# Kernel tuning notes

Measured on AMD Instinct MI355X. Metric: run time of the kernel, lower is better.

## Reference

```python
import jax, jax.numpy as jnp
from jax import lax
import numpy as np

B, CIN, CP, H, W = 16, 64, 64, 64, 64
K1 = 3   # deformable kernel
K2 = 5   # parallel conv kernel
EPS = 1e-5


def conv2d(x, w, stride, pad):
    return lax.conv_general_dilated(
        x, w, (stride, stride), [(pad, pad), (pad, pad)],
        dimension_numbers=('NCHW', 'OIHW', 'NCHW'))


def batchnorm(x, g, b, m, v):
    scale = g / jnp.sqrt(v + EPS)
    return (x - m[None, :, None, None]) * scale[None, :, None, None] + b[None, :, None, None]


def deform_conv2d(x, offset, weight, stride, pad):
    # x: [B,Cin,H,W], offset: [B,2*K*K,Ho,Wo] (dy,dx interleaved per kernel tap, torchvision layout)
    Bn, Cin, Hn, Wn = x.shape
    Cout, _, K, _ = weight.shape
    KK = K * K
    Ho, Wo = offset.shape[2], offset.shape[3]
    off = offset.reshape(Bn, KK, 2, Ho, Wo)
    dy, dx = off[:, :, 0], off[:, :, 1]                      # [B,KK,Ho,Wo]
    ky, kx = jnp.meshgrid(jnp.arange(K), jnp.arange(K), indexing='ij')
    ky = ky.reshape(KK).astype(x.dtype)
    kx = kx.reshape(KK).astype(x.dtype)
    base_y = (jnp.arange(Ho) * stride - pad).astype(x.dtype)
    base_x = (jnp.arange(Wo) * stride - pad).astype(x.dtype)
    ys = base_y[None, None, :, None] + ky[None, :, None, None] + dy  # [B,KK,Ho,Wo]
    xs = base_x[None, None, None, :] + kx[None, :, None, None] + dx
    y0 = jnp.floor(ys); x0 = jnp.floor(xs)
    wy1 = ys - y0; wx1 = xs - x0
    wy0 = 1.0 - wy1; wx0 = 1.0 - wx1
    flat = x.reshape(Bn, Cin, Hn * Wn)

    def gather(yi, xi):
        valid = ((yi >= 0) & (yi <= Hn - 1) & (xi >= 0) & (xi <= Wn - 1))
        yc = jnp.clip(yi, 0, Hn - 1).astype(jnp.int32)
        xc = jnp.clip(xi, 0, Wn - 1).astype(jnp.int32)
        idx = (yc * Wn + xc).reshape(Bn, -1)                 # [B,KK*Ho*Wo]
        g = jax.vmap(lambda f, i: jnp.take(f, i, axis=1))(flat, idx)
        g = g.reshape(Bn, Cin, KK, Ho, Wo)
        return g * valid.astype(x.dtype)[:, None]

    val = (gather(y0, x0) * (wy0 * wx0)[:, None]
           + gather(y0, x0 + 1) * (wy0 * wx1)[:, None]
           + gather(y0 + 1, x0) * (wy1 * wx0)[:, None]
           + gather(y0 + 1, x0 + 1) * (wy1 * wx1)[:, None])   # [B,Cin,KK,Ho,Wo]
    w_r = weight.reshape(Cout, Cin, KK)
    return jnp.einsum('bcknm,ock->bonm', val, w_r)


def setup_inputs():
    key = jax.random.key(0)
    ks = jax.random.split(key, 18)
    f32 = jnp.float32
    x = jax.random.normal(ks[0], (B, CIN, H, W), f32)
    w_off = jax.random.normal(ks[1], (2 * K1 * K1, CIN, 3, 3), f32) * 0.01
    b_off = jnp.zeros((2 * K1 * K1,), f32)
    w1 = jax.random.normal(ks[2], (CP, CIN, K1, K1), f32) / np.sqrt(CIN * K1 * K1)
    w3 = jax.random.normal(ks[3], (CP, CIN, K2, K2), f32) / np.sqrt(CIN * K2 * K2)
    w2 = jax.random.normal(ks[4], (CP, CP, 3, 3), f32) / np.sqrt(CP * 9)
    def bn(i):
        g = jax.random.uniform(ks[5 + 4 * i], (CP,), f32, 0.5, 1.5)
        b = jax.random.normal(ks[6 + 4 * i], (CP,), f32) * 0.1
        m = jax.random.normal(ks[7 + 4 * i], (CP,), f32) * 0.1
        v = jax.random.uniform(ks[8 + 4 * i], (CP,), f32, 0.5, 1.5)
        return g, b, m, v
    g1, b1, m1, v1 = bn(0)
    g3, b3, m3, v3 = bn(1)
    g2, b2, m2, v2 = bn(2)
    return dict(x=x, w_off=w_off, b_off=b_off, w1=w1, g1=g1, b1=b1, m1=m1, v1=v1,
                w3=w3, g3=g3, b3=b3, m3=m3, v3=v3, w2=w2, g2=g2, b2=b2, m2=m2, v2=v2)


def reference(x, w_off, b_off, w1, g1, b1, m1, v1, w3, g3, b3, m3, v3, w2, g2, b2, m2, v2):
    offset1 = conv2d(x, w_off, 1, 1) + b_off[None, :, None, None]
    out = jax.nn.relu(batchnorm(deform_conv2d(x, offset1, w1, 1, 1), g1, b1, m1, v1))
    out_1 = jax.nn.relu(batchnorm(conv2d(x, w3, 1, 2), g3, b3, m3, v3))
    out = out + out_1
    out = batchnorm(conv2d(out, w2, 1, 1), g2, b2, m2, v2)
    out = out + x  # identity shortcut (stride=1, in_planes==planes)
    return jax.nn.relu(out)
```

## Files before the change

### kernel.cpp

```cpp
#include <hip/hip_runtime.h>
#include <hip/hip_bf16.h>


#define EPSv 1e-5f
#define XP 68

typedef _Float16 f16x2 __attribute__((ext_vector_type(2)));
typedef _Float16 f16x8 __attribute__((ext_vector_type(8)));
typedef __attribute__((ext_vector_type(16))) float f32x16;

__device__ inline ushort f2h(float f) {
  _Float16 h = (_Float16)f;
  return *(ushort*)&h;
}

__global__ __launch_bounds__(256) void prep_kernel(
    const float* __restrict__ x, const float* __restrict__ w3,
    const float* __restrict__ w2, const float* __restrict__ w1,
    const float* __restrict__ w_off,
    ushort* __restrict__ xTp, ushort* __restrict__ w3F,
    ushort* __restrict__ w2F, ushort* __restrict__ w1F,
    ushort* __restrict__ wofF) {
  __shared__ float tile[64][65];
  const int blk = blockIdx.x;
  if (blk < 1024) {
    const int y = blk & 63, b = blk >> 6;
    for (int i = threadIdx.x; i < 4096; i += 256) {
      int ci = i >> 6, xx = i & 63;
      tile[ci][xx] = x[(((size_t)b * 64 + ci) * 64 + y) * 64 + xx];
    }
    __syncthreads();
    for (int i = threadIdx.x; i < 2048; i += 256) {
      int xx = i >> 5, cip = (i & 31) * 2;
      ushort2 v;
      v.x = f2h(tile[cip][xx]);
      v.y = f2h(tile[cip + 1][xx]);
      *(ushort2*)&xTp[(((size_t)(b * 64 + y) * XP) + (xx + 2)) * 64 + cip] = v;
    }
    if (threadIdx.x < 128) {
      int colid = threadIdx.x >> 5;
      int col = (colid & 1) + (colid >> 1) * 66;
      int cip = (threadIdx.x & 31) * 2;
      ushort2 z; z.x = 0; z.y = 0;
      *(ushort2*)&xTp[(((size_t)(b * 64 + y) * XP) + col) * 64 + cip] = z;
    }
    return;
  }
  int idx = (blk - 1024) * 256 + threadIdx.x;
  if (idx < 102400) {
    int j = idx & 7, lane = (idx >> 3) & 63, ks = (idx >> 9) & 3;
    int half = (idx >> 11) & 1, kk = idx >> 12;
    int ln = lane & 31, kh = lane >> 5;
    int co = half * 32 + ln, ci = ks * 16 + kh * 8 + j;
    w3F[idx] = f2h(w3[(co * 64 + ci) * 25 + kk]);
    return;
  }
  idx -= 102400;
  if (idx < 36864) {
    int j = idx & 7, lane = (idx >> 3) & 63, ks = (idx >> 9) & 3;
    int half = (idx >> 11) & 1, kk = idx >> 12;
    int ln = lane & 31, kh = lane >> 5;
    int co = half * 32 + ln, ci = ks * 16 + kh * 8 + j;
    w2F[idx] = f2h(w2[(co * 64 + ci) * 9 + kk]);
    return;
  }
  idx -= 36864;
  if (idx < 36864) {
    int j = idx & 7, lane = (idx >> 3) & 63, ks = (idx >> 9) & 3;
    int half = (idx >> 11) & 1, kk = idx >> 12;
    int ln = lane & 31, kh = lane >> 5;
    int co = half * 32 + ln, ci = ks * 16 + kh * 8 + j;
    w1F[idx] = f2h(w1[(co * 64 + ci) * 9 + kk]);
    return;
  }
  idx -= 36864;
  if (idx < 18432) {
    int j = idx & 7, lane = (idx >> 3) & 63, ks = (idx >> 9) & 3;
    int kk = idx >> 11;
    int ln = lane & 31, kh = lane >> 5;
    int ci = ks * 16 + kh * 8 + j;
    wofF[idx] = f2h(ln < 18 ? w_off[(ln * 64 + ci) * 9 + kk] : 0.f);
  }
}

__device__ __forceinline__ f16x8 blend4(f16x8 va, f16x8 vb, f16x8 vc, f16x8 vd,
                                        f16x2 w00, f16x2 w01, f16x2 w10, f16x2 w11) {
  const f16x2* a = (const f16x2*)&va;
  const f16x2* b = (const f16x2*)&vb;
  const f16x2* c = (const f16x2*)&vc;
  const f16x2* d = (const f16x2*)&vd;
  f16x8 f;
  f16x2* fo = (f16x2*)&f;
#pragma unroll
  for (int i = 0; i < 4; ++i)
    fo[i] = a[i] * w00 + b[i] * w01 + c[i] * w10 + d[i] * w11;
  return f;
}

__global__ __launch_bounds__(256, 2) void fused_kernel(
    const ushort* __restrict__ xTp, const ushort* __restrict__ wofF,
    const float* __restrict__ b_off, const ushort* __restrict__ w1F,
    const ushort* __restrict__ w3F,
    const float* __restrict__ g1, const float* __restrict__ b1,
    const float* __restrict__ m1, const float* __restrict__ v1,
    const float* __restrict__ g3, const float* __restrict__ b3,
    const float* __restrict__ m3, const float* __restrict__ v3,
    ushort* __restrict__ s1T) {
  __shared__ __align__(16) uint4 ldsx[6 * 68 * 8];
  __shared__ float bn1s[64], bn1b[64], bn3s[64], bn3b[64];

  const int tid = threadIdx.x;
  const int wv = tid >> 6, lane = tid & 63;
  const int ln = lane & 31, kh = lane >> 5;
  const int r = wv >> 1, nt = wv & 1;
  const int y0 = blockIdx.x * 2, b = blockIdx.y;
  const int y = y0 + r, px = nt * 32 + ln;
  const uint4* xT4 = (const uint4*)xTp;
  const ushort* xb = xTp + (size_t)b * 64 * XP * 64;
  const bool interior = (y0 >= 2 && y0 <= 60);

  if (tid < 64) {
    float s = g1[tid] * rsqrtf(v1[tid] + EPSv);
    bn1s[tid] = s; bn1b[tid] = b1[tid] - m1[tid] * s;
    float s3 = g3[tid] * rsqrtf(v3[tid] + EPSv);
    bn3s[tid] = s3; bn3b[tid] = b3[tid] - m3[tid] * s3;
  }
  for (int i = tid; i < 6 * 68 * 8; i += 256) {
    int tr = i / (68 * 8), rem = i % (68 * 8);
    int col = rem >> 3, c = rem & 7;
    int ysrc = min(max(y0 - 2 + tr, 0), 63);
    uint4 v = xT4[((size_t)((b * 64 + ysrc) * XP + col)) * 8 + c];
    ldsx[(tr * 68 + col) * 8 + (c ^ (col & 7))] = v;
  }
  __syncthreads();

  f32x16 acco;
#pragma unroll
  for (int j = 0; j < 16; ++j) acco[j] = 0.f;
  if (interior) {
#pragma unroll
    for (int kk = 0; kk < 9; ++kk) {
      const int ky = kk / 3, kx = kk % 3;
      const int tr = r + ky + 1;
      const int col = px + kx + 1;
      f16x8 af[4], bf[4];
#pragma unroll
      for (int ks = 0; ks < 4; ++ks)
        af[ks] = *(const f16x8*)&wofF[(size_t)((kk * 4 + ks) * 64 + lane) * 8];
#pragma unroll
      for (int ks = 0; ks < 4; ++ks) {
        int c = ks * 2 + kh;
        bf[ks] = *(const f16x8*)&ldsx[(tr * 68 + col) * 8 + (c ^ (col & 7))];
      }
#pragma unroll
      for (int ks = 0; ks < 4; ++ks)
        acco = __builtin_amdgcn_mfma_f32_32x32x16_f16(af[ks], bf[ks], acco, 0, 0, 0);
    }
  } else {
#pragma unroll
    for (int kk = 0; kk < 9; ++kk) {
      const int ky = kk / 3, kx = kk % 3;
      const int yy = y - 1 + ky;
      if (yy >= 0 && yy <= 63) {
        const int tr = yy - (y0 - 2);
        const int col = px + kx + 1;
#pragma unroll
        for (int ks = 0; ks < 4; ++ks) {
          int c = ks * 2 + kh;
          f16x8 af = *(const f16x8*)&wofF[(size_t)((kk * 4 + ks) * 64 + lane) * 8];
          f16x8 bf = *(const f16x8*)&ldsx[(tr * 68 + col) * 8 + (c ^ (col & 7))];
          acco = __builtin_amdgcn_mfma_f32_32x32x16_f16(af, bf, acco, 0, 0, 0);
        }
      }
    }
  }
  float oth[10];
#pragma unroll
  for (int t = 0; t < 10; ++t) oth[t] = __shfl_xor(acco[t], 32);
  float dyv[9], dxv[9];
#pragma unroll
  for (int kk = 0; kk < 9; ++kk) {
    const int cY = 2 * kk, cX = 2 * kk + 1;
    const int rY = (cY & 3) + 4 * (cY >> 3);
    const int rX = (cX & 3) + 4 * (cX >> 3);
    const int sY = (cY >> 2) & 1, sX = (cX >> 2) & 1;
    float vy = (sY == kh) ? acco[rY] : oth[rY];
    float vx = (sX == kh) ? acco[rX] : oth[rX];
    dyv[kk] = vy + b_off[cY];
    dxv[kk] = vx + b_off[cX];
  }
  bool fast = true;
#pragma unroll
  for (int kk = 0; kk < 9; ++kk) {
    int iy0 = (int)floorf((float)(y - 1 + kk / 3) + dyv[kk]);
    int iy1 = iy0 + 1;
    bool ok0 = (iy0 < 0) || (iy0 > 63) || (iy0 >= y0 - 2 && iy0 <= y0 + 3);
    bool ok1 = (iy1 < 0) || (iy1 > 63) || (iy1 >= y0 - 2 && iy1 <= y0 + 3);
    fast = fast && ok0 && ok1;
  }
  const bool allfast = (__ballot(!fast) == 0ull);

  f32x16 accd0, accd1, acc50, acc51;
#pragma unroll
  for (int j = 0; j < 16; ++j) {
    accd0[j] = 0.f; accd1[j] = 0.f; acc50[j] = 0.f; acc51[j] = 0.f;
  }

  if (interior && allfast) {
#pragma unroll
    for (int dk = 0; dk < 9; ++dk) {
      {
        const int ky = dk / 3, kx = dk % 3;
        float ys = (float)(y - 1 + ky) + dyv[dk];
        float xs = (float)(px - 1 + kx) + dxv[dk];
        float y0f = floorf(ys), x0f = floorf(xs);
        float wy1 = ys - y0f, wx1 = xs - x0f;
        float wy0 = 1.f - wy1, wx0 = 1.f - wx1;
        int iy0 = (int)y0f, ix0 = (int)x0f;
        int iy1 = iy0 + 1, ix1 = ix0 + 1;
        float vy0 = (iy0 >= 0 && iy0 <= 63) ? 1.f : 0.f;
        float vy1 = (iy1 >= 0 && iy1 <= 63) ? 1.f : 0.f;
        float vx0 = (ix0 >= 0 && ix0 <= 63) ? 1.f : 0.f;
        float vx1 = (ix1 >= 0 && ix1 <= 63) ? 1.f : 0.f;
        int x0c = min(max(ix0, 0), 63), x1c = min(max(ix1, 0), 63);
        float w00 = wy0 * wx0 * vy0 * vx0;
        float w01 = wy0 * wx1 * vy0 * vx1;
        float w10 = wy1 * wx0 * vy1 * vx0;
        float w11 = wy1 * wx1 * vy1 * vx1;
        int tr0 = min(max(iy0 - (y0 - 2), 0), 5);
        int tr1 = min(max(iy1 - (y0 - 2), 0), 5);
        int c0 = x0c + 2, c1 = x1c + 2;
        f16x2 w00v = {(_Float16)w00, (_Float16)w00};
        f16x2 w01v = {(_Float16)w01, (_Float16)w01};
        f16x2 w10v = {(_Float16)w10, (_Float16)w10};
        f16x2 w11v = {(_Float16)w11, (_Float16)w11};

        f16x8 a0[4], a1[4], va[4], vb[4], vc[4], vd[4];
#pragma unroll
        for (int ks = 0; ks < 4; ++ks) {
          a0[ks] = *(const f16x8*)&w1F[(size_t)(((dk * 2 + 0) * 4 + ks) * 64 + lane) * 8];
          a1[ks] = *(const f16x8*)&w1F[(size_t)(((dk * 2 + 1) * 4 + ks) * 64 + lane) * 8];
        }
#pragma unroll
        for (int ks = 0; ks < 4; ++ks) {
          int c = ks * 2 + kh;
          va[ks] = *(const f16x8*)&ldsx[(tr0 * 68 + c0) * 8 + (c ^ (c0 & 7))];
          vb[ks] = *(const f16x8*)&ldsx[(tr0 * 68 + c1) * 8 + (c ^ (c1 & 7))];
          vc[ks] = *(const f16x8*)&ldsx[(tr1 * 68 + c0) * 8 + (c ^ (c0 & 7))];
          vd[ks] = *(const f16x8*)&ldsx[(tr1 * 68 + c1) * 8 + (c ^ (c1 & 7))];
        }
#pragma unroll
        for (int ks = 0; ks < 4; ++ks) {
          f16x8 f = blend4(va[ks], vb[ks], vc[ks], vd[ks], w00v, w01v, w10v, w11v);
          accd0 = __builtin_amdgcn_mfma_f32_32x32x16_f16(a0[ks], f, accd0, 0, 0, 0);
          accd1 = __builtin_amdgcn_mfma_f32_32x32x16_f16(a1[ks], f, accd1, 0, 0, 0);
        }
      }
      const int n5 = (dk < 7) ? 3 : 2;
      const int b5 = (dk < 7) ? dk * 3 : 21 + (dk - 7) * 2;
#pragma unroll
      for (int t = 0; t < 3; ++t) {
        if (t < n5) {
          const int kk = b5 + t;
          const int ky5 = kk / 5, kx5 = kk % 5;
          const int tr = r + ky5;
          const int col = px + kx5;
          f16x8 a0[4], a1[4], bfv[4];
#pragma unroll
          for (int ks = 0; ks < 4; ++ks) {
            a0[ks] = *(const f16x8*)&w3F[(size_t)(((kk * 2 + 0) * 4 + ks) * 64 + lane) * 8];
            a1[ks] = *(const f16x8*)&w3F[(size_t)(((kk * 2 + 1) * 4 + ks) * 64 + lane) * 8];
          }
#pragma unroll
          for (int ks = 0; ks < 4; ++ks) {
            int c = ks * 2 + kh;
            bfv[ks] = *(const f16x8*)&ldsx[(tr * 68 + col) * 8 + (c ^ (col & 7))];
          }
#pragma unroll
          for (int ks = 0; ks < 4; ++ks) {
            acc50 = __builtin_amdgcn_mfma_f32_32x32x16_f16(a0[ks], bfv[ks], acc50, 0, 0, 0);
            acc51 = __builtin_amdgcn_mfma_f32_32x32x16_f16(a1[ks], bfv[ks], acc51, 0, 0, 0);
          }
        }
      }
    }
  } else {
    if (allfast) {
#pragma unroll
      for (int kk = 0; kk < 9; ++kk) {
        const int ky = kk / 3, kx = kk % 3;
        float ys = (float)(y - 1 + ky) + dyv[kk];
        float xs = (float)(px - 1 + kx) + dxv[kk];
        float y0f = floorf(ys), x0f = floorf(xs);
        float wy1 = ys - y0f, wx1 = xs - x0f;
        float wy0 = 1.f - wy1, wx0 = 1.f - wx1;
        int iy0 = (int)y0f, ix0 = (int)x0f;
        int iy1 = iy0 + 1, ix1 = ix0 + 1;
        float vy0 = (iy0 >= 0 && iy0 <= 63) ? 1.f : 0.f;
        float vy1 = (iy1 >= 0 && iy1 <= 63) ? 1.f : 0.f;
        float vx0 = (ix0 >= 0 && ix0 <= 63) ? 1.f : 0.f;
        float vx1 = (ix1 >= 0 && ix1 <= 63) ? 1.f : 0.f;
        int x0c = min(max(ix0, 0), 63), x1c = min(max(ix1, 0), 63);
        float w00 = wy0 * wx0 * vy0 * vx0;
        float w01 = wy0 * wx1 * vy0 * vx1;
        float w10 = wy1 * wx0 * vy1 * vx0;
        float w11 = wy1 * wx1 * vy1 * vx1;
        int tr0 = min(max(iy0 - (y0 - 2), 0), 5);
        int tr1 = min(max(iy1 - (y0 - 2), 0), 5);
        int c0 = x0c + 2, c1 = x1c + 2;
        f16x2 w00v = {(_Float16)w00, (_Float16)w00};
        f16x2 w01v = {(_Float16)w01, (_Float16)w01};
        f16x2 w10v = {(_Float16)w10, (_Float16)w10};
        f16x2 w11v = {(_Float16)w11, (_Float16)w11};
#pragma unroll
        for (int ks = 0; ks < 4; ++ks) {
          int c = ks * 2 + kh;
          f16x8 va = *(const f16x8*)&ldsx[(tr0 * 68 + c0) * 8 + (c ^ (c0 & 7))];
          f16x8 vb = *(const f16x8*)&ldsx[(tr0 * 68 + c1) * 8 + (c ^ (c1 & 7))];
          f16x8 vc = *(const f16x8*)&ldsx[(tr1 * 68 + c0) * 8 + (c ^ (c0 & 7))];
          f16x8 vd = *(const f16x8*)&ldsx[(tr1 * 68 + c1) * 8 + (c ^ (c1 & 7))];
          f16x8 f = blend4(va, vb, vc, vd, w00v, w01v, w10v, w11v);
          f16x8 a0 = *(const f16x8*)&w1F[(size_t)(((kk * 2 + 0) * 4 + ks) * 64 + lane) * 8];
          f16x8 a1 = *(const f16x8*)&w1F[(size_t)(((kk * 2 + 1) * 4 + ks) * 64 + lane) * 8];
          accd0 = __builtin_amdgcn_mfma_f32_32x32x16_f16(a0, f, accd0, 0, 0, 0);
          accd1 = __builtin_amdgcn_mfma_f32_32x32x16_f16(a1, f, accd1, 0, 0, 0);
        }
      }
    } else {
#pragma unroll
      for (int kk = 0; kk < 9; ++kk) {
        const int ky = kk / 3, kx = kk % 3;
        float ys = (float)(y - 1 + ky) + dyv[kk];
        float xs = (float)(px - 1 + kx) + dxv[kk];
        float y0f = floorf(ys), x0f = floorf(xs);
        float wy1 = ys - y0f, wx1 = xs - x0f;
        float wy0 = 1.f - wy1, wx0 = 1.f - wx1;
        int iy0 = (int)y0f, ix0 = (int)x0f;
        int iy1 = iy0 + 1, ix1 = ix0 + 1;
        float vy0 = (iy0 >= 0 && iy0 <= 63) ? 1.f : 0.f;
        float vy1 = (iy1 >= 0 && iy1 <= 63) ? 1.f : 0.f;
        float vx0 = (ix0 >= 0 && ix0 <= 63) ? 1.f : 0.f;
        float vx1 = (ix1 >= 0 && ix1 <= 63) ? 1.f : 0.f;
        int x0c = min(max(ix0, 0), 63), x1c = min(max(ix1, 0), 63);
        int y0c = min(max(iy0, 0), 63), y1c = min(max(iy1, 0), 63);
        float w00 = wy0 * wx0 * vy0 * vx0;
        float w01 = wy0 * wx1 * vy0 * vx1;
        float w10 = wy1 * wx0 * vy1 * vx0;
        float w11 = wy1 * wx1 * vy1 * vx1;
        int tr0 = min(max(iy0 - (y0 - 2), 0), 5);
        int tr1 = min(max(iy1 - (y0 - 2), 0), 5);
        int c0 = x0c + 2, c1 = x1c + 2;
        f16x2 w00v = {(_Float16)w00, (_Float16)w00};
        f16x2 w01v = {(_Float16)w01, (_Float16)w01};
        f16x2 w10v = {(_Float16)w10, (_Float16)w10};
        f16x2 w11v = {(_Float16)w11, (_Float16)w11};

        f16x8 frag[4];
#pragma unroll
        for (int ks = 0; ks < 4; ++ks) {
          int c = ks * 2 + kh;
          f16x8 va = *(const f16x8*)&ldsx[(tr0 * 68 + c0) * 8 + (c ^ (c0 & 7))];
          f16x8 vb = *(const f16x8*)&ldsx[(tr0 * 68 + c1) * 8 + (c ^ (c1 & 7))];
          f16x8 vc = *(const f16x8*)&ldsx[(tr1 * 68 + c0) * 8 + (c ^ (c0 & 7))];
          f16x8 vd = *(const f16x8*)&ldsx[(tr1 * 68 + c1) * 8 + (c ^ (c1 & 7))];
          frag[ks] = blend4(va, vb, vc, vd, w00v, w01v, w10v, w11v);
        }
        if (!fast) {
          const ushort* p00 = xb + ((size_t)(y0c * XP + x0c + 2)) * 64 + kh * 8;
          const ushort* p01 = xb + ((size_t)(y0c * XP + x1c + 2)) * 64 + kh * 8;
          const ushort* p10 = xb + ((size_t)(y1c * XP + x0c + 2)) * 64 + kh * 8;
          const ushort* p11 = xb + ((size_t)(y1c * XP + x1c + 2)) * 64 + kh * 8;
#pragma unroll
          for (int ks = 0; ks < 4; ++ks) {
            f16x8 va = *(const f16x8*)(p00 + ks * 16);
            f16x8 vb = *(const f16x8*)(p01 + ks * 16);
            f16x8 vc = *(const f16x8*)(p10 + ks * 16);
            f16x8 vd = *(const f16x8*)(p11 + ks * 16);
            frag[ks] = blend4(va, vb, vc, vd, w00v, w01v, w10v, w11v);
          }
        }
#pragma unroll
        for (int ks = 0; ks < 4; ++ks) {
          f16x8 a0 = *(const f16x8*)&w1F[(size_t)(((kk * 2 + 0) * 4 + ks) * 64 + lane) * 8];
          f16x8 a1 = *(const f16x8*)&w1F[(size_t)(((kk * 2 + 1) * 4 + ks) * 64 + lane) * 8];
          accd0 = __builtin_amdgcn_mfma_f32_32x32x16_f16(a0, frag[ks], accd0, 0, 0, 0);
          accd1 = __builtin_amdgcn_mfma_f32_32x32x16_f16(a1, frag[ks], accd1, 0, 0, 0);
        }
      }
    }
    if (interior) {
#pragma unroll
      for (int kk = 0; kk < 25; ++kk) {
        const int ky = kk / 5, kx = kk % 5;
        const int tr = r + ky;
        const int col = px + kx;
        f16x8 a0[4], a1[4], bfv[4];
#pragma unroll
        for (int ks = 0; ks < 4; ++ks) {
          a0[ks] = *(const f16x8*)&w3F[(size_t)(((kk * 2 + 0) * 4 + ks) * 64 + lane) * 8];
          a1[ks] = *(const f16x8*)&w3F[(size_t)(((kk * 2 + 1) * 4 + ks) * 64 + lane) * 8];
        }
#pragma unroll
        for (int ks = 0; ks < 4; ++ks) {
          int c = ks * 2 + kh;
          bfv[ks] = *(const f16x8*)&ldsx[(tr * 68 + col) * 8 + (c ^ (col & 7))];
        }
#pragma unroll
        for (int ks = 0; ks < 4; ++ks) {
          acc50 = __builtin_amdgcn_mfma_f32_32x32x16_f16(a0[ks], bfv[ks], acc50, 0, 0, 0);
          acc51 = __builtin_amdgcn_mfma_f32_32x32x16_f16(a1[ks], bfv[ks], acc51, 0, 0, 0);
        }
      }
    } else {
#pragma unroll
      for (int kk = 0; kk < 25; ++kk) {
        const int ky = kk / 5, kx = kk % 5;
        const int yy = y - 2 + ky;
        if (yy >= 0 && yy <= 63) {
          const int tr = r + ky;
          const int col = px + kx;
#pragma unroll
          for (int ks = 0; ks < 4; ++ks) {
            int c = ks * 2 + kh;
            f16x8 bf = *(const f16x8*)&ldsx[(tr * 68 + col) * 8 + (c ^ (col & 7))];
            f16x8 a0 = *(const f16x8*)&w3F[(size_t)(((kk * 2 + 0) * 4 + ks) * 64 + lane) * 8];
            f16x8 a1 = *(const f16x8*)&w3F[(size_t)(((kk * 2 + 1) * 4 + ks) * 64 + lane) * 8];
            acc50 = __builtin_amdgcn_mfma_f32_32x32x16_f16(a0, bf, acc50, 0, 0, 0);
            acc51 = __builtin_amdgcn_mfma_f32_32x32x16_f16(a1, bf, acc51, 0, 0, 0);
          }
        }
      }
    }
  }

  ushort* op = s1T + ((size_t)((b * 64 + y) * 64 + px)) * 64;
#pragma unroll
  for (int q = 0; q < 4; ++q) {
    int co0 = 8 * q + 4 * kh;
    float vv[4];
#pragma unroll
    for (int rr = 0; rr < 4; ++rr) {
      int co = co0 + rr;
      float vd = accd0[q * 4 + rr] * bn1s[co] + bn1b[co];
      vd = vd > 0.f ? vd : 0.f;
      float v5 = acc50[q * 4 + rr] * bn3s[co] + bn3b[co];
      v5 = v5 > 0.f ? v5 : 0.f;
      vv[rr] = vd + v5;
    }
    ushort4 st;
    st.x = f2h(vv[0]); st.y = f2h(vv[1]); st.z = f2h(vv[2]); st.w = f2h(vv[3]);
    *(ushort4*)(op + co0) = st;
#pragma unroll
    for (int rr = 0; rr < 4; ++rr) {
      int co = co0 + 32 + rr;
      float vd = accd1[q * 4 + rr] * bn1s[co] + bn1b[co];
      vd = vd > 0.f ? vd : 0.f;
      float v5 = acc51[q * 4 + rr] * bn3s[co] + bn3b[co];
      v5 = v5 > 0.f ? v5 : 0.f;
      vv[rr] = vd + v5;
    }
    st.x = f2h(vv[0]); st.y = f2h(vv[1]); st.z = f2h(vv[2]); st.w = f2h(vv[3]);
    *(ushort4*)(op + co0 + 32) = st;
  }
}

__global__ __launch_bounds__(256, 2) void conv3_mfma_kernel(
    const ushort* __restrict__ s1T, const ushort* __restrict__ w2F,
    const float* __restrict__ g2, const float* __restrict__ b2,
    const float* __restrict__ m2, const float* __restrict__ v2,
    const float* __restrict__ x, float* __restrict__ out) {
  __shared__ __align__(16) uint4 Bt[3 * 66 * 8];
  __shared__ float sc[64], bi[64];
  const int tid = threadIdx.x;
  if (tid < 64) {
    float s = g2[tid] * rsqrtf(v2[tid] + EPSv);
    sc[tid] = s;
    bi[tid] = b2[tid] - m2[tid] * s;
  }
  const int y = blockIdx.x, b = blockIdx.y;
  const int wv = tid >> 6, lane = tid & 63;
  const int ln = lane & 31, kh = lane >> 5;
  const int mh = wv & 1, nt = wv >> 1;
  const int px = nt * 32 + ln;
  const uint4* s1T4 = (const uint4*)s1T;

  for (int i = tid; i < 3 * 66 * 8; i += 256) {
    int tr = i / (66 * 8), rem = i % (66 * 8);
    int col = rem >> 3, c = rem & 7;
    int yy = y - 1 + tr, xcol = col - 1;
    uint4 v = make_uint4(0, 0, 0, 0);
    if (yy >= 0 && yy <= 63 && xcol >= 0 && xcol <= 63)
      v = s1T4[((size_t)((b * 64 + yy) * 64 + xcol)) * 8 + c];
    Bt[(tr * 66 + col) * 8 + (c ^ (col & 7))] = v;
  }
  __syncthreads();

  f32x16 acc;
#pragma unroll
  for (int j = 0; j < 16; ++j) acc[j] = 0.f;

#pragma unroll
  for (int kk = 0; kk < 9; ++kk) {
    const int ky = kk / 3, kx = kk % 3;
    const int col = px + kx;
    f16x8 af[4], bfr[4];
#pragma unroll
    for (int ccb = 0; ccb < 4; ++ccb)
      af[ccb] = *(const f16x8*)&w2F[(size_t)(((kk * 2 + mh) * 4 + ccb) * 64 + lane) * 8];
#pragma unroll
    for (int ccb = 0; ccb < 4; ++ccb) {
      int c = ccb * 2 + kh;
      bfr[ccb] = *(const f16x8*)&Bt[(ky * 66 + col) * 8 + (c ^ (col & 7))];
    }
#pragma unroll
    for (int ccb = 0; ccb < 4; ++ccb)
      acc = __builtin_amdgcn_mfma_f32_32x32x16_f16(af[ccb], bfr[ccb], acc, 0, 0, 0);
  }
#pragma unroll
  for (int reg = 0; reg < 16; ++reg) {
    int co = (reg & 3) + 8 * (reg >> 2) + 4 * kh + mh * 32;
    size_t o = (((size_t)b * 64 + co) * 64 + y) * 64 + px;
    float v = acc[reg] * sc[co] + bi[co] + x[o];
    out[o] = v > 0.f ? v : 0.f;
  }
}

extern "C" void kernel_launch(void* const* d_in, const int* in_sizes, int n_in,
                              void* d_out, int out_size, void* d_ws, size_t ws_size,
                              hipStream_t stream) {
  const float* x     = (const float*)d_in[0];
  const float* w_off = (const float*)d_in[1];
  const float* b_off = (const float*)d_in[2];
  const float* w1    = (const float*)d_in[3];
  const float* g1    = (const float*)d_in[4];
  const float* b1    = (const float*)d_in[5];
  const float* m1    = (const float*)d_in[6];
  const float* v1    = (const float*)d_in[7];
  const float* w3    = (const float*)d_in[8];
  const float* g3    = (const float*)d_in[9];
  const float* b3    = (const float*)d_in[10];
  const float* m3    = (const float*)d_in[11];
  const float* v3    = (const float*)d_in[12];
  const float* w2    = (const float*)d_in[13];
  const float* g2    = (const float*)d_in[14];
  const float* b2    = (const float*)d_in[15];
  const float* m2    = (const float*)d_in[16];
  const float* v2    = (const float*)d_in[17];
  float* out = (float*)d_out;

  ushort* xTp  = (ushort*)d_ws;
  ushort* s1T  = xTp + (size_t)16 * 64 * XP * 64;
  ushort* w3F  = s1T + (size_t)16 * 64 * 64 * 64;
  ushort* w2F  = w3F + 102400;
  ushort* w1F  = w2F + 36864;
  ushort* wofF = w1F + 36864;

  prep_kernel<<<dim3(1024 + 760), dim3(256), 0, stream>>>(x, w3, w2, w1, w_off,
                                                          xTp, w3F, w2F, w1F, wofF);
  fused_kernel<<<dim3(32, 16), dim3(256), 0, stream>>>(xTp, wofF, b_off, w1F, w3F,
                                                       g1, b1, m1, v1, g3, b3, m3, v3,
                                                       s1T);
  conv3_mfma_kernel<<<dim3(64, 16), dim3(256), 0, stream>>>(s1T, w2F, g2, b2, m2, v2,
                                                            x, out);
}
```

Baseline: 62.54 us.

## Split fused kernel into deform and 5x5 conv wave roles with LDS accumulator exchange

```diff
diff --git a/kernel.cpp b/kernel.cpp
--- a/kernel.cpp
+++ b/kernel.cpp
@@ -97,7 +97,7 @@
   return f;
 }
 
-__global__ __launch_bounds__(256, 2) void fused_kernel(
+__global__ __launch_bounds__(512, 4) void fused_kernel(
     const ushort* __restrict__ xTp, const ushort* __restrict__ wofF,
     const float* __restrict__ b_off, const ushort* __restrict__ w1F,
     const ushort* __restrict__ w3F,
@@ -112,7 +112,7 @@
   const int tid = threadIdx.x;
   const int wv = tid >> 6, lane = tid & 63;
   const int ln = lane & 31, kh = lane >> 5;
-  const int r = wv >> 1, nt = wv & 1;
+  const int role = wv >> 2, r = (wv >> 1) & 1, nt = wv & 1;
   const int y0 = blockIdx.x * 2, b = blockIdx.y;
   const int y = y0 + r, px = nt * 32 + ln;
   const uint4* xT4 = (const uint4*)xTp;
@@ -125,7 +125,7 @@
     float s3 = g3[tid] * rsqrtf(v3[tid] + EPSv);
     bn3s[tid] = s3; bn3b[tid] = b3[tid] - m3[tid] * s3;
   }
-  for (int i = tid; i < 6 * 68 * 8; i += 256) {
+  for (int i = tid; i < 6 * 68 * 8; i += 512) {
     int tr = i / (68 * 8), rem = i % (68 * 8);
     int col = rem >> 3, c = rem & 7;
     int ysrc = min(max(y0 - 2 + tr, 0), 63);
@@ -134,35 +134,19 @@
   }
   __syncthreads();
 
-  f32x16 acco;
-#pragma unroll
-  for (int j = 0; j < 16; ++j) acco[j] = 0.f;
-  if (interior) {
-#pragma unroll
-    for (int kk = 0; kk < 9; ++kk) {
-      const int ky = kk / 3, kx = kk % 3;
-      const int tr = r + ky + 1;
-      const int col = px + kx + 1;
-      f16x8 af[4], bf[4];
-#pragma unroll
-      for (int ks = 0; ks < 4; ++ks)
-        af[ks] = *(const f16x8*)&wofF[(size_t)((kk * 4 + ks) * 64 + lane) * 8];
-#pragma unroll
-      for (int ks = 0; ks < 4; ++ks) {
-        int c = ks * 2 + kh;
-        bf[ks] = *(const f16x8*)&ldsx[(tr * 68 + col) * 8 + (c ^ (col & 7))];
-      }
-#pragma unroll
-      for (int ks = 0; ks < 4; ++ks)
-        acco = __builtin_amdgcn_mfma_f32_32x32x16_f16(af[ks], bf[ks], acco, 0, 0, 0);
-    }
-  } else {
-#pragma unroll
-    for (int kk = 0; kk < 9; ++kk) {
-      const int ky = kk / 3, kx = kk % 3;
-      const int yy = y - 1 + ky;
-      if (yy >= 0 && yy <= 63) {
-        const int tr = yy - (y0 - 2);
+  f32x16 accKeep, accGive;
+#pragma unroll
+  for (int j = 0; j < 16; ++j) { accKeep[j] = 0.f; accGive[j] = 0.f; }
+
+  if (role == 0) {
+    f32x16 acco;
+#pragma unroll
+    for (int j = 0; j < 16; ++j) acco[j] = 0.f;
+    if (interior) {
+#pragma unroll
+      for (int kk = 0; kk < 9; ++kk) {
+        const int ky = kk / 3, kx = kk % 3;
+        const int tr = r + ky + 1;
         const int col = px + kx + 1;
 #pragma unroll
         for (int ks = 0; ks < 4; ++ks) {
@@ -172,120 +156,50 @@
           acco = __builtin_amdgcn_mfma_f32_32x32x16_f16(af, bf, acco, 0, 0, 0);
         }
       }
-    }
-  }
-  float oth[10];
-#pragma unroll
-  for (int t = 0; t < 10; ++t) oth[t] = __shfl_xor(acco[t], 32);
-  float dyv[9], dxv[9];
-#pragma unroll
-  for (int kk = 0; kk < 9; ++kk) {
-    const int cY = 2 * kk, cX = 2 * kk + 1;
-    const int rY = (cY & 3) + 4 * (cY >> 3);
-    const int rX = (cX & 3) + 4 * (cX >> 3);
-    const int sY = (cY >> 2) & 1, sX = (cX >> 2) & 1;
-    float vy = (sY == kh) ? acco[rY] : oth[rY];
-    float vx = (sX == kh) ? acco[rX] : oth[rX];
-    dyv[kk] = vy + b_off[cY];
-    dxv[kk] = vx + b_off[cX];
-  }
-  bool fast = true;
-#pragma unroll
-  for (int kk = 0; kk < 9; ++kk) {
-    int iy0 = (int)floorf((float)(y - 1 + kk / 3) + dyv[kk]);
-    int iy1 = iy0 + 1;
-    bool ok0 = (iy0 < 0) || (iy0 > 63) || (iy0 >= y0 - 2 && iy0 <= y0 + 3);
-    bool ok1 = (iy1 < 0) || (iy1 > 63) || (iy1 >= y0 - 2 && iy1 <= y0 + 3);
-    fast = fast && ok0 && ok1;
-  }
-  const bool allfast = (__ballot(!fast) == 0ull);
-
-  f32x16 accd0, accd1, acc50, acc51;
-#pragma unroll
-  for (int j = 0; j < 16; ++j) {
-    accd0[j] = 0.f; accd1[j] = 0.f; acc50[j] = 0.f; acc51[j] = 0.f;
-  }
-
-  if (interior && allfast) {
-#pragma unroll
-    for (int dk = 0; dk < 9; ++dk) {
-      {
-        const int ky = dk / 3, kx = dk % 3;
-        float ys = (float)(y - 1 + ky) + dyv[dk];
-        float xs = (float)(px - 1 + kx) + dxv[dk];
-        float y0f = floorf(ys), x0f = floorf(xs);
-        float wy1 = ys - y0f, wx1 = xs - x0f;
-        float wy0 = 1.f - wy1, wx0 = 1.f - wx1;
-        int iy0 = (int)y0f, ix0 = (int)x0f;
-        int iy1 = iy0 + 1, ix1 = ix0 + 1;
-        float vy0 = (iy0 >= 0 && iy0 <= 63) ? 1.f : 0.f;
-        float vy1 = (iy1 >= 0 && iy1 <= 63) ? 1.f : 0.f;
-        float vx0 = (ix0 >= 0 && ix0 <= 63) ? 1.f : 0.f;
-        float vx1 = (ix1 >= 0 && ix1 <= 63) ? 1.f : 0.f;
-        int x0c = min(max(ix0, 0), 63), x1c = min(max(ix1, 0), 63);
-        float w00 = wy0 * wx0 * vy0 * vx0;
-        float w01 = wy0 * wx1 * vy0 * vx1;
-        float w10 = wy1 * wx0 * vy1 * vx0;
-        float w11 = wy1 * wx1 * vy1 * vx1;
-        int tr0 = min(max(iy0 - (y0 - 2), 0), 5);
-        int tr1 = min(max(iy1 - (y0 - 2), 0), 5);
-        int c0 = x0c + 2, c1 = x1c + 2;
-        f16x2 w00v = {(_Float16)w00, (_Float16)w00};
-        f16x2 w01v = {(_Float16)w01, (_Float16)w01};
-        f16x2 w10v = {(_Float16)w10, (_Float16)w10};
-        f16x2 w11v = {(_Float16)w11, (_Float16)w11};
-
-        f16x8 a0[4], a1[4], va[4], vb[4], vc[4], vd[4];
-#pragma unroll
-        for (int ks = 0; ks < 4; ++ks) {
-          a0[ks] = *(const f16x8*)&w1F[(size_t)(((dk * 2 + 0) * 4 + ks) * 64 + lane) * 8];
-          a1[ks] = *(const f16x8*)&w1F[(size_t)(((dk * 2 + 1) * 4 + ks) * 64 + lane) * 8];
-        }
-#pragma unroll
-        for (int ks = 0; ks < 4; ++ks) {
-          int c = ks * 2 + kh;
-          va[ks] = *(const f16x8*)&ldsx[(tr0 * 68 + c0) * 8 + (c ^ (c0 & 7))];
-          vb[ks] = *(const f16x8*)&ldsx[(tr0 * 68 + c1) * 8 + (c ^ (c1 & 7))];
-          vc[ks] = *(const f16x8*)&ldsx[(tr1 * 68 + c0) * 8 + (c ^ (c0 & 7))];
-          vd[ks] = *(const f16x8*)&ldsx[(tr1 * 68 + c1) * 8 + (c ^ (c1 & 7))];
-        }
-#pragma unroll
-        for (int ks = 0; ks < 4; ++ks) {
-          f16x8 f = blend4(va[ks], vb[ks], vc[ks], vd[ks], w00v, w01v, w10v, w11v);
-          accd0 = __builtin_amdgcn_mfma_f32_32x32x16_f16(a0[ks], f, accd0, 0, 0, 0);
-          accd1 = __builtin_amdgcn_mfma_f32_32x32x16_f16(a1[ks], f, accd1, 0, 0, 0);
-        }
-      }
-      const int n5 = (dk < 7) ? 3 : 2;
-      const int b5 = (dk < 7) ? dk * 3 : 21 + (dk - 7) * 2;
-#pragma unroll
-      for (int t = 0; t < 3; ++t) {
-        if (t < n5) {
-          const int kk = b5 + t;
-          const int ky5 = kk / 5, kx5 = kk % 5;
-          const int tr = r + ky5;
-          const int col = px + kx5;
-          f16x8 a0[4], a1[4], bfv[4];
-#pragma unroll
-          for (int ks = 0; ks < 4; ++ks) {
-            a0[ks] = *(const f16x8*)&w3F[(size_t)(((kk * 2 + 0) * 4 + ks) * 64 + lane) * 8];
-            a1[ks] = *(const f16x8*)&w3F[(size_t)(((kk * 2 + 1) * 4 + ks) * 64 + lane) * 8];
-          }
+    } else {
+#pragma unroll
+      for (int kk = 0; kk < 9; ++kk) {
+        const int ky = kk / 3, kx = kk % 3;
+        const int yy = y - 1 + ky;
+        if (yy >= 0 && yy <= 63) {
+          const int tr = yy - (y0 - 2);
+          const int col = px + kx + 1;
 #pragma unroll
           for (int ks = 0; ks < 4; ++ks) {
             int c = ks * 2 + kh;
-            bfv[ks] = *(const f16x8*)&ldsx[(tr * 68 + col) * 8 + (c ^ (col & 7))];
+            f16x8 af = *(const f16x8*)&wofF[(size_t)((kk * 4 + ks) * 64 + lane) * 8];
+            f16x8 bf = *(const f16x8*)&ldsx[(tr * 68 + col) * 8 + (c ^ (col & 7))];
+            acco = __builtin_amdgcn_mfma_f32_32x32x16_f16(af, bf, acco, 0, 0, 0);
           }
-#pragma unroll
-          for (int ks = 0; ks < 4; ++ks) {
-            acc50 = __builtin_amdgcn_mfma_f32_32x32x16_f16(a0[ks], bfv[ks], acc50, 0, 0, 0);
-            acc51 = __builtin_amdgcn_mfma_f32_32x32x16_f16(a1[ks], bfv[ks], acc51, 0, 0, 0);
-          }
-        }
-      }
-    }
-  } else {
-    if (allfast) {
+        }
+      }
+    }
+    float oth[10];
+#pragma unroll
+    for (int t = 0; t < 10; ++t) oth[t] = __shfl_xor(acco[t], 32);
+    float dyv[9], dxv[9];
+#pragma unroll
+    for (int kk = 0; kk < 9; ++kk) {
+      const int cY = 2 * kk, cX = 2 * kk + 1;
+      const int rY = (cY & 3) + 4 * (cY >> 3);
+      const int rX = (cX & 3) + 4 * (cX >> 3);
+      const int sY = (cY >> 2) & 1, sX = (cX >> 2) & 1;
+      float vy = (sY == kh) ? acco[rY] : oth[rY];
+      float vx = (sX == kh) ? acco[rX] : oth[rX];
+      dyv[kk] = vy + b_off[cY];
+      dxv[kk] = vx + b_off[cX];
+    }
+    bool fast = true;
+#pragma unroll
+    for (int kk = 0; kk < 9; ++kk) {
+      int iy0 = (int)floorf((float)(y - 1 + kk / 3) + dyv[kk]);
+      int iy1 = iy0 + 1;
+      bool ok0 = (iy0 < 0) || (iy0 > 63) || (iy0 >= y0 - 2 && iy0 <= y0 + 3);
+      bool ok1 = (iy1 < 0) || (iy1 > 63) || (iy1 >= y0 - 2 && iy1 <= y0 + 3);
+      fast = fast && ok0 && ok1;
+    }
+
+    if (__ballot(!fast) == 0ull) {
 #pragma unroll
       for (int kk = 0; kk < 9; ++kk) {
         const int ky = kk / 3, kx = kk % 3;
@@ -322,8 +236,8 @@
           f16x8 f = blend4(va, vb, vc, vd, w00v, w01v, w10v, w11v);
           f16x8 a0 = *(const f16x8*)&w1F[(size_t)(((kk * 2 + 0) * 4 + ks) * 64 + lane) * 8];
           f16x8 a1 = *(const f16x8*)&w1F[(size_t)(((kk * 2 + 1) * 4 + ks) * 64 + lane) * 8];
-          accd0 = __builtin_amdgcn_mfma_f32_32x32x16_f16(a0, f, accd0, 0, 0, 0);
-          accd1 = __builtin_amdgcn_mfma_f32_32x32x16_f16(a1, f, accd1, 0, 0, 0);
+          accKeep = __builtin_amdgcn_mfma_f32_32x32x16_f16(a0, f, accKeep, 0, 0, 0);
+          accGive = __builtin_amdgcn_mfma_f32_32x32x16_f16(a1, f, accGive, 0, 0, 0);
         }
       }
     } else {
@@ -383,11 +297,12 @@
         for (int ks = 0; ks < 4; ++ks) {
           f16x8 a0 = *(const f16x8*)&w1F[(size_t)(((kk * 2 + 0) * 4 + ks) * 64 + lane) * 8];
           f16x8 a1 = *(const f16x8*)&w1F[(size_t)(((kk * 2 + 1) * 4 + ks) * 64 + lane) * 8];
-          accd0 = __builtin_amdgcn_mfma_f32_32x32x16_f16(a0, frag[ks], accd0, 0, 0, 0);
-          accd1 = __builtin_amdgcn_mfma_f32_32x32x16_f16(a1, frag[ks], accd1, 0, 0, 0);
-        }
-      }
-    }
+          accKeep = __builtin_amdgcn_mfma_f32_32x32x16_f16(a0, frag[ks], accKeep, 0, 0, 0);
+          accGive = __builtin_amdgcn_mfma_f32_32x32x16_f16(a1, frag[ks], accGive, 0, 0, 0);
+        }
+      }
+    }
+  } else {
     if (interior) {
 #pragma unroll
       for (int kk = 0; kk < 25; ++kk) {
@@ -407,8 +322,8 @@
         }
 #pragma unroll
         for (int ks = 0; ks < 4; ++ks) {
-          acc50 = __builtin_amdgcn_mfma_f32_32x32x16_f16(a0[ks], bfv[ks], acc50, 0, 0, 0);
-          acc51 = __builtin_amdgcn_mfma_f32_32x32x16_f16(a1[ks], bfv[ks], acc51, 0, 0, 0);
+          accGive = __builtin_amdgcn_mfma_f32_32x32x16_f16(a0[ks], bfv[ks], accGive, 0, 0, 0);
+          accKeep = __builtin_amdgcn_mfma_f32_32x32x16_f16(a1[ks], bfv[ks], accKeep, 0, 0, 0);
         }
       }
     } else {
@@ -425,42 +340,49 @@
             f16x8 bf = *(const f16x8*)&ldsx[(tr * 68 + col) * 8 + (c ^ (col & 7))];
             f16x8 a0 = *(const f16x8*)&w3F[(size_t)(((kk * 2 + 0) * 4 + ks) * 64 + lane) * 8];
             f16x8 a1 = *(const f16x8*)&w3F[(size_t)(((kk * 2 + 1) * 4 + ks) * 64 + lane) * 8];
-            acc50 = __builtin_amdgcn_mfma_f32_32x32x16_f16(a0, bf, acc50, 0, 0, 0);
-            acc51 = __builtin_amdgcn_mfma_f32_32x32x16_f16(a1, bf, acc51, 0, 0, 0);
+            accGive = __builtin_amdgcn_mfma_f32_32x32x16_f16(a0, bf, accGive, 0, 0, 0);
+            accKeep = __builtin_amdgcn_mfma_f32_32x32x16_f16(a1, bf, accKeep, 0, 0, 0);
           }
         }
       }
     }
   }
 
-  ushort* op = s1T + ((size_t)((b * 64 + y) * 64 + px)) * 64;
-#pragma unroll
-  for (int q = 0; q < 4; ++q) {
-    int co0 = 8 * q + 4 * kh;
-    float vv[4];
-#pragma unroll
-    for (int rr = 0; rr < 4; ++rr) {
-      int co = co0 + rr;
-      float vd = accd0[q * 4 + rr] * bn1s[co] + bn1b[co];
-      vd = vd > 0.f ? vd : 0.f;
-      float v5 = acc50[q * 4 + rr] * bn3s[co] + bn3b[co];
-      v5 = v5 > 0.f ? v5 : 0.f;
-      vv[rr] = vd + v5;
-    }
-    ushort4 st;
-    st.x = f2h(vv[0]); st.y = f2h(vv[1]); st.z = f2h(vv[2]); st.w = f2h(vv[3]);
-    *(ushort4*)(op + co0) = st;
-#pragma unroll
-    for (int rr = 0; rr < 4; ++rr) {
-      int co = co0 + 32 + rr;
-      float vd = accd1[q * 4 + rr] * bn1s[co] + bn1b[co];
-      vd = vd > 0.f ? vd : 0.f;
-      float v5 = acc51[q * 4 + rr] * bn3s[co] + bn3b[co];
-      v5 = v5 > 0.f ? v5 : 0.f;
-      vv[rr] = vd + v5;
-    }
-    st.x = f2h(vv[0]); st.y = f2h(vv[1]); st.z = f2h(vv[2]); st.w = f2h(vv[3]);
-    *(ushort4*)(op + co0 + 32) = st;
+  __syncthreads();
+  {
+    float4* sp = (float4*)ldsx;
+    const int base = (wv & 3) * 8;
+    union U { f32x16 v; float4 q[4]; };
+    U give, got;
+    give.v = accGive;
+    const int wbase = base + role * 4;
+#pragma unroll
+    for (int j = 0; j < 4; ++j) sp[(size_t)(wbase + j) * 64 + lane] = give.q[j];
+    __syncthreads();
+    const int rbase = base + 4 - role * 4;
+#pragma unroll
+    for (int j = 0; j < 4; ++j) got.q[j] = sp[(size_t)(rbase + j) * 64 + lane];
+
+    f32x16 vdacc = (role == 0) ? accKeep : got.v;
+    f32x16 v5acc = (role == 0) ? got.v : accKeep;
+    ushort* op = s1T + ((size_t)((b * 64 + y) * 64 + px)) * 64 + role * 32;
+#pragma unroll
+    for (int q = 0; q < 4; ++q) {
+      int co0 = role * 32 + 8 * q + 4 * kh;
+      float vv[4];
+#pragma unroll
+      for (int rr = 0; rr < 4; ++rr) {
+        int co = co0 + rr;
+        float vd = vdacc[q * 4 + rr] * bn1s[co] + bn1b[co];
+        vd = vd > 0.f ? vd : 0.f;
+        float v5 = v5acc[q * 4 + rr] * bn3s[co] + bn3b[co];
+        v5 = v5 > 0.f ? v5 : 0.f;
+        vv[rr] = vd + v5;
+      }
+      ushort4 st;
+      st.x = f2h(vv[0]); st.y = f2h(vv[1]); st.z = f2h(vv[2]); st.w = f2h(vv[3]);
+      *(ushort4*)(op + 8 * q + 4 * kh) = st;
+    }
   }
 }
 
@@ -557,7 +479,7 @@
 
   prep_kernel<<<dim3(1024 + 760), dim3(256), 0, stream>>>(x, w3, w2, w1, w_off,
                                                           xTp, w3F, w2F, w1F, wofF);
-  fused_kernel<<<dim3(32, 16), dim3(256), 0, stream>>>(xTp, wofF, b_off, w1F, w3F,
+  fused_kernel<<<dim3(32, 16), dim3(512), 0, stream>>>(xTp, wofF, b_off, w1F, w3F,
                                                        g1, b1, m1, v1, g3, b3, m3, v3,
                                                        s1T);
   conv3_mfma_kernel<<<dim3(64, 16), dim3(256), 0, stream>>>(s1T, w2F, g2, b2, m2, v2,
```

Result: slower. 65.49 us (+4.7%).
